# Optimization experiments

Hardware: AMD Instinct MI355X
Metric: run time of the kernel (lower is better)

The kernel has to match this reference:

```python
import jax, jax.numpy as jnp
import numpy as np
from jax import lax

VOCAB = 32000
EMB = 512
HID = 1024
BATCH = 64
MAX_LEN = 30
STEPS = MAX_LEN + 2
SOS = 1
PAD = 0


def setup_inputs() -> dict:
    key = jax.random.key(0)
    ks = jax.random.split(key, 9)
    s = 0.05
    target = jax.random.randint(ks[0], (BATCH, 1), 0, VOCAB)
    encoder_hidden = jax.random.normal(ks[1], (1, BATCH, HID), dtype=jnp.float32)
    emb = jax.random.normal(ks[2], (VOCAB, EMB), dtype=jnp.float32) * s
    emb = emb.at[PAD].set(0.0)  # padding_idx row zeroed like torch
    W_ih = jax.random.normal(ks[3], (3 * HID, EMB), dtype=jnp.float32) * s
    W_hh = jax.random.normal(ks[4], (3 * HID, HID), dtype=jnp.float32) * s
    b_ih = jax.random.normal(ks[5], (3 * HID,), dtype=jnp.float32) * s
    b_hh = jax.random.normal(ks[6], (3 * HID,), dtype=jnp.float32) * s
    fc_W = jax.random.normal(ks[7], (VOCAB, HID), dtype=jnp.float32) * s
    fc_b = jax.random.normal(ks[8], (VOCAB,), dtype=jnp.float32) * s
    return {"target": target, "encoder_hidden": encoder_hidden, "emb": emb,
            "W_ih": W_ih, "W_hh": W_hh, "b_ih": b_ih, "b_hh": b_hh,
            "fc_W": fc_W, "fc_b": fc_b}


def reference(target, encoder_hidden, emb, W_ih, W_hh, b_ih, b_hh, fc_W, fc_b):
    B = target.shape[0]

    def step(carry, _):
        tok, h = carry                      # tok [B] int, h [B,H]
        x = emb[tok]                        # [B,E] embedding lookup
        gi = x @ W_ih.T + b_ih              # [B,3H]
        gh = h @ W_hh.T + b_hh              # [B,3H]
        i_r, i_z, i_n = jnp.split(gi, 3, axis=-1)
        h_r, h_z, h_n = jnp.split(gh, 3, axis=-1)
        r = jax.nn.sigmoid(i_r + h_r)
        z = jax.nn.sigmoid(i_z + h_z)
        n = jnp.tanh(i_n + r * h_n)
        h_new = (1.0 - z) * n + z * h       # torch GRU update
        logits = h_new @ fc_W.T + fc_b      # [B,V]
        logp = jax.nn.log_softmax(logits, axis=-1)
        tok_new = jnp.argmax(logp, axis=-1)  # greedy feedback (topk, k=1)
        return (tok_new, h_new), logp

    h0 = encoder_hidden[0]                  # num_layers == 1
    tok0 = jnp.full((B,), SOS, dtype=jnp.int32)
    (_, hT), outs = lax.scan(step, (tok0, h0), None, length=STEPS)
    decoder_outputs = jnp.transpose(outs, (1, 0, 2))  # [B, STEPS, V]
    return decoder_outputs, hT[None]
```

## Files before the change

kernel.cpp:

```cpp
#include <hip/hip_runtime.h>

#define VV 32000
#define EE 512
#define HH 1024
#define NB 64
#define NSTEP 32

typedef __attribute__((ext_vector_type(8))) short short8;
typedef __attribute__((ext_vector_type(4))) float f32x4;
typedef unsigned long long u64;

#define MFMA16(a, b, c) __builtin_amdgcn_mfma_f32_16x16x32_bf16((a), (b), (c), 0, 0, 0)

__device__ __forceinline__ unsigned short f2bf(float f) {
  unsigned int u = __float_as_uint(f);
  u += 0x7fffu + ((u >> 16) & 1u);
  return (unsigned short)(u >> 16);
}
__device__ __forceinline__ float bf2f(unsigned short b) {
  return __uint_as_float(((unsigned int)b) << 16);
}
__device__ __forceinline__ float sigmoidf_(float x) { return 1.0f / (1.0f + expf(-x)); }
__device__ __forceinline__ unsigned int ordkey(float f) {
  unsigned int u = __float_as_uint(f);
  return u ^ ((u >> 31) ? 0xFFFFFFFFu : 0x80000000u);
}
__device__ __forceinline__ float ordkey_inv(unsigned int u) {
  return __uint_as_float((u & 0x80000000u) ? (u ^ 0x80000000u) : ~u);
}

__global__ __launch_bounds__(256) void prep_wcat(const float* __restrict__ Wih,
                                                 const float* __restrict__ Whh,
                                                 unsigned short* __restrict__ wm,
                                                 unsigned short* __restrict__ wr) {
  int ub = blockIdx.x / 3, g = blockIdx.x % 3;
  for (int e = threadIdx.x; e < 48 * 64; e += 256) {
    int ks = e >> 6, lane = e & 63;
    int row = g * HH + ub * 16 + (lane & 15);
    int k0 = ks * 32 + ((lane >> 4) << 3);
    const float* srcp = (k0 < EE) ? (Wih + (size_t)row * EE + k0)
                                  : (Whh + (size_t)row * HH + (k0 - EE));
    float4 f0 = ((const float4*)srcp)[0];
    float4 f1 = ((const float4*)srcp)[1];
    float fs[8] = {f0.x, f0.y, f0.z, f0.w, f1.x, f1.y, f1.z, f1.w};
    short8 om, orr;
#pragma unroll
    for (int j = 0; j < 8; ++j) {
      unsigned short m_ = f2bf(fs[j]);
      om[j] = (short)m_;
      orr[j] = (short)f2bf(fs[j] - bf2f(m_));
    }
    size_t o8 = ((size_t)(ub * 3 + g) * 48 + ks) * 64 + lane;
    ((short8*)wm)[o8] = om;
    ((short8*)wr)[o8] = orr;
  }
}

__global__ __launch_bounds__(256) void prep_wfc(const float* __restrict__ fcW,
                                                unsigned short* __restrict__ wfc) {
  int vg = blockIdx.x;
  for (int e = threadIdx.x; e < 4096; e += 256) {
    int ks = e >> 7, n = (e >> 6) & 1, lane = e & 63;
    int v = vg * 32 + n * 16 + (lane & 15);
    int k0 = ks * 32 + ((lane >> 4) << 3);
    const float4* src = (const float4*)(fcW + (size_t)v * HH + k0);
    float4 f0 = src[0];
    float4 f1 = src[1];
    float fs[8] = {f0.x, f0.y, f0.z, f0.w, f1.x, f1.y, f1.z, f1.w};
    short8 o;
#pragma unroll
    for (int j = 0; j < 8; ++j) o[j] = (short)f2bf(fs[j]);
    ((short8*)wfc)[(size_t)((vg * 32 + ks) * 2 + n) * 64 + lane] = o;
  }
}

__global__ __launch_bounds__(256) void init_kernel(
    const float* __restrict__ enc, const float* __restrict__ emb, float* __restrict__ h4a,
    unsigned short* __restrict__ ham, unsigned short* __restrict__ har,
    unsigned short* __restrict__ xam, unsigned short* __restrict__ xar,
    int* __restrict__ cnt, int* __restrict__ arrive) {
  int i = blockIdx.x * 256 + threadIdx.x;
  int b = i >> 10, u = i & 1023;
  float hv = enc[i];
  h4a[i] = hv;
  unsigned short m_ = f2bf(hv);
  size_t idx = (((size_t)(b >> 4) * 32 + (u >> 5)) * 64 + ((b & 15) + (((u >> 3) & 3) << 4))) * 8 + (u & 7);
  ham[idx] = m_;
  har[idx] = f2bf(hv - bf2f(m_));
  if (i < NB * EE) {
    int b2 = i >> 9, k = i & 511;
    float xv = emb[EE + k];
    unsigned short xm = f2bf(xv);
    size_t xi = (((size_t)(b2 >> 4) * 16 + (k >> 5)) * 64 + ((b2 & 15) + (((k >> 3) & 3) << 4))) * 8 + (k & 7);
    xam[xi] = xm;
    xar[xi] = f2bf(xv - bf2f(xm));
  }
  if (i < NB) { cnt[i] = 0; arrive[i] = 0; }
}

__global__ __launch_bounds__(768, 3) void gru_kernel(
    const unsigned short* __restrict__ xam, const unsigned short* __restrict__ xar,
    const unsigned short* __restrict__ him, const unsigned short* __restrict__ hir,
    const float* __restrict__ h4in, float* __restrict__ h4out,
    const unsigned short* __restrict__ wm, const unsigned short* __restrict__ wrs,
    const float* __restrict__ bih, const float* __restrict__ bhh,
    unsigned short* __restrict__ hom, unsigned short* __restrict__ hor) {
  __shared__ float red[12][16][65];
  const int tid = threadIdx.x, lane = tid & 63, w = tid >> 6;
  const int ub = blockIdx.x >> 2, mg = blockIdx.x & 3;
  f32x4 aR{}, aZ{}, aNX{}, aNH{};
  const short8* XM = (const short8*)xam;
  const short8* XR = (const short8*)xar;
  const short8* HM = (const short8*)him;
  const short8* HR = (const short8*)hir;
  const short8* WM = (const short8*)wm;
  const short8* WR = (const short8*)wrs;
#pragma unroll
  for (int s = 0; s < 4; ++s) {
    int ks = w * 4 + s;
    short8 am, ar;
    if (ks < 16) {
      int o = (mg * 16 + ks) * 64 + lane;
      am = XM[o]; ar = XR[o];
    } else {
      int o = (mg * 32 + (ks - 16)) * 64 + lane;
      am = HM[o]; ar = HR[o];
    }
    {
      int o = ((ub * 3 + 0) * 48 + ks) * 64 + lane;
      short8 wmv = WM[o], wrv = WR[o];
      aR = MFMA16(am, wmv, aR); aR = MFMA16(ar, wmv, aR); aR = MFMA16(am, wrv, aR);
    }
    {
      int o = ((ub * 3 + 1) * 48 + ks) * 64 + lane;
      short8 wmv = WM[o], wrv = WR[o];
      aZ = MFMA16(am, wmv, aZ); aZ = MFMA16(ar, wmv, aZ); aZ = MFMA16(am, wrv, aZ);
    }
    {
      int o = ((ub * 3 + 2) * 48 + ks) * 64 + lane;
      short8 wmv = WM[o], wrv = WR[o];
      if (ks < 16) {
        aNX = MFMA16(am, wmv, aNX); aNX = MFMA16(ar, wmv, aNX); aNX = MFMA16(am, wrv, aNX);
      } else {
        aNH = MFMA16(am, wmv, aNH); aNH = MFMA16(ar, wmv, aNH); aNH = MFMA16(am, wrv, aNH);
      }
    }
  }
#pragma unroll
  for (int reg = 0; reg < 4; ++reg) {
    int rr = ((lane >> 4) << 2) + reg, c = lane & 15;
    red[w][rr][c] = aR[reg];
    red[w][rr][16 + c] = aZ[reg];
    red[w][rr][32 + c] = aNX[reg];
    red[w][rr][48 + c] = aNH[reg];
  }
  __syncthreads();
  if (tid < 256) {
    const int mrow = tid >> 4, uu = tid & 15;
    float R = 0.f, Z = 0.f, NX = 0.f, NH = 0.f;
#pragma unroll
    for (int q = 0; q < 12; ++q) {
      R += red[q][mrow][uu];
      Z += red[q][mrow][16 + uu];
      NX += red[q][mrow][32 + uu];
      NH += red[q][mrow][48 + uu];
    }
    const int b = mg * 16 + mrow, u = ub * 16 + uu;
    float r = sigmoidf_(R + bih[u] + bhh[u]);
    float z = sigmoidf_(Z + bih[HH + u] + bhh[HH + u]);
    float n = tanhf(NX + bih[2 * HH + u] + r * (NH + bhh[2 * HH + u]));
    float hold = h4in[b * HH + u];
    float hn = (1.0f - z) * n + z * hold;
    h4out[b * HH + u] = hn;
    unsigned short m_ = f2bf(hn);
    size_t idx = (((size_t)(b >> 4) * 32 + (u >> 5)) * 64 + ((b & 15) + (((u >> 3) & 3) << 4))) * 8 + (u & 7);
    hom[idx] = m_;
    hor[idx] = f2bf(hn - bf2f(m_));
  }
}

__global__ __launch_bounds__(256, 8) void fc_kernel(
    const unsigned short* __restrict__ ham,
    const unsigned short* __restrict__ wfc, const float* __restrict__ fcb,
    unsigned short* __restrict__ lgb, u64* __restrict__ blkkeys, int t) {
  const int tid = threadIdx.x;
  const int lane = tid & 63, w = tid >> 6;
  const int vg = blockIdx.x;
  f32x4 acc0{}, acc1{};
  const short8* HM = (const short8*)ham + (size_t)w * 2048;
  const short8* W = (const short8*)wfc + (size_t)vg * 4096;
#pragma unroll 8
  for (int ks = 0; ks < 32; ++ks) {
    short8 am = HM[ks * 64 + lane];
    short8 w0 = W[(ks * 2 + 0) * 64 + lane];
    short8 w1 = W[(ks * 2 + 1) * 64 + lane];
    acc0 = MFMA16(am, w0, acc0);
    acc1 = MFMA16(am, w1, acc1);
  }
  const int r0 = lane >> 4, c0 = lane & 15;
  const float b0 = fcb[vg * 32 + c0];
  const float b1 = fcb[vg * 32 + 16 + c0];
  u64 kk[4];
#pragma unroll
  for (int reg = 0; reg < 4; ++reg) {
    const int b = w * 16 + r0 * 4 + reg;
    float v0 = acc0[reg] + b0;
    float v1 = acc1[reg] + b1;
    size_t ro = ((size_t)b * NSTEP + t) * VV + (size_t)vg * 32 + c0;
    lgb[ro] = f2bf(v0);
    lgb[ro + 16] = f2bf(v1);
    u64 k0 = ((u64)ordkey(v0) << 32) | (u64)(0xFFFFFFFFu - (unsigned)(vg * 32 + c0));
    u64 k1 = ((u64)ordkey(v1) << 32) | (u64)(0xFFFFFFFFu - (unsigned)(vg * 32 + 16 + c0));
    kk[reg] = k0 > k1 ? k0 : k1;
  }
#pragma unroll
  for (int d = 1; d < 16; d <<= 1)
#pragma unroll
    for (int reg = 0; reg < 4; ++reg) {
      u64 o = __shfl_xor(kk[reg], d, 64);
      if (o > kk[reg]) kk[reg] = o;
    }
  if (c0 == 0) {
#pragma unroll
    for (int reg = 0; reg < 4; ++reg)
      blkkeys[(size_t)(w * 16 + r0 * 4 + reg) * 1000 + vg] = kk[reg];
  }
}

__global__ __launch_bounds__(256) void sel_kernel(
    const unsigned short* __restrict__ lgb, const u64* __restrict__ blkkeys,
    int* __restrict__ cnt, int* __restrict__ cand, int* __restrict__ arrive,
    const float* __restrict__ fcW, const float* __restrict__ fcb,
    const float* __restrict__ emb, const float* __restrict__ h4,
    unsigned short* __restrict__ xam, unsigned short* __restrict__ xar, int t) {
  const int b = blockIdx.x >> 3, q = blockIdx.x & 7;
  const int tid = threadIdx.x;
  __shared__ u64 skey[256];
  __shared__ int slast, stok;
  __shared__ u64 rkey[256];

  const u64* kb = blkkeys + (size_t)b * 1000;
  u64 mk = 0;
  for (int i = tid; i < 1000; i += 256) {
    u64 k = kb[i];
    if (k > mk) mk = k;
  }
  skey[tid] = mk;
  __syncthreads();
  for (int off = 128; off > 0; off >>= 1) {
    if (tid < off && skey[tid + off] > skey[tid]) skey[tid] = skey[tid + off];
    __syncthreads();
  }
  const float Mf = ordkey_inv((unsigned)(skey[0] >> 32));
  const float thr = Mf - 0.10f;

  const short8* r8v = (const short8*)(lgb + ((size_t)b * NSTEP + t) * VV);
  for (int i = q * 500 + tid; i < (q + 1) * 500; i += 256) {
    short8 v8 = r8v[i];
#pragma unroll
    for (int e = 0; e < 8; ++e) {
      float x = bf2f((unsigned short)v8[e]);
      if (x >= thr) {
        int p = atomicAdd(&cnt[b], 1);
        if (p < 256) atomicExch(&cand[b * 256 + p], i * 8 + e);
      }
    }
  }
  __syncthreads();
  if (tid == 0) slast = (atomicAdd(&arrive[b], 1) == 7) ? 1 : 0;
  __syncthreads();
  if (!slast) return;

  int n = atomicAdd(&cnt[b], 0);
  if (n > 256) n = 256;
  const int w = tid >> 6, ln = tid & 63;
  for (int ci = w; ci < n; ci += 4) {
    int v = atomicAdd(&cand[b * 256 + ci], 0);
    float p = 0.f;
#pragma unroll
    for (int qq = 0; qq < 16; ++qq)
      p += h4[b * HH + ln + (qq << 6)] * fcW[(size_t)v * HH + ln + (qq << 6)];
#pragma unroll
    for (int d = 1; d < 64; d <<= 1) p += __shfl_xor(p, d);
    if (ln == 0)
      rkey[ci] = ((u64)ordkey(p + fcb[v]) << 32) | (u64)(0xFFFFFFFFu - (unsigned)v);
  }
  __syncthreads();
  if (tid == 0) {
    u64 bk = 0;
    for (int ci = 0; ci < n; ++ci)
      if (rkey[ci] > bk) bk = rkey[ci];
    stok = (int)(0xFFFFFFFFu - (unsigned)(bk & 0xFFFFFFFFu));
    atomicExch(&cnt[b], 0);
    atomicExch(&arrive[b], 0);
  }
  __syncthreads();

  const int tok = stok;
  for (int k = tid; k < EE; k += 256) {
    float xv = emb[(size_t)tok * EE + k];
    unsigned short xm = f2bf(xv);
    size_t xi = (((size_t)(b >> 4) * 16 + (k >> 5)) * 64 + ((b & 15) + (((k >> 3) & 3) << 4))) * 8 + (k & 7);
    xam[xi] = xm;
    xar[xi] = f2bf(xv - bf2f(xm));
  }
}

__global__ __launch_bounds__(256) void lsm_kernel(const unsigned short* __restrict__ lgb,
                                                  const float* __restrict__ h4,
                                                  float* __restrict__ out) {
  const int bid = blockIdx.x;
  const int tid = threadIdx.x;
  if (bid >= 2048) {
    int i = (bid - 2048) * 256 + tid;
    out[(size_t)NB * NSTEP * VV + i] = h4[i];
    return;
  }
  const short8* r8v = (const short8*)(lgb + (size_t)bid * VV);
  float* orow = out + (size_t)bid * VV;
  __shared__ float mred[256], sred[256];

  float m = -INFINITY;
  for (int i = tid; i < VV / 8; i += 256) {
    short8 v8 = r8v[i];
    float m0 = fmaxf(bf2f((unsigned short)v8[0]), bf2f((unsigned short)v8[1]));
    float m1 = fmaxf(bf2f((unsigned short)v8[2]), bf2f((unsigned short)v8[3]));
    float m2 = fmaxf(bf2f((unsigned short)v8[4]), bf2f((unsigned short)v8[5]));
    float m3 = fmaxf(bf2f((unsigned short)v8[6]), bf2f((unsigned short)v8[7]));
    m = fmaxf(m, fmaxf(fmaxf(m0, m1), fmaxf(m2, m3)));
  }
  mred[tid] = m;
  __syncthreads();
  for (int off = 128; off > 0; off >>= 1) {
    if (tid < off) mred[tid] = fmaxf(mred[tid], mred[tid + off]);
    __syncthreads();
  }
  const float M = mred[0];

  float s0 = 0.f, s1 = 0.f, s2 = 0.f, s3 = 0.f;
  for (int i = tid; i < VV / 8; i += 256) {
    short8 v8 = r8v[i];
    s0 += __expf(bf2f((unsigned short)v8[0]) - M) + __expf(bf2f((unsigned short)v8[4]) - M);
    s1 += __expf(bf2f((unsigned short)v8[1]) - M) + __expf(bf2f((unsigned short)v8[5]) - M);
    s2 += __expf(bf2f((unsigned short)v8[2]) - M) + __expf(bf2f((unsigned short)v8[6]) - M);
    s3 += __expf(bf2f((unsigned short)v8[3]) - M) + __expf(bf2f((unsigned short)v8[7]) - M);
  }
  sred[tid] = (s0 + s1) + (s2 + s3);
  __syncthreads();
  for (int off = 128; off > 0; off >>= 1) {
    if (tid < off) sred[tid] += sred[tid + off];
    __syncthreads();
  }
  const float lse = M + logf(sred[0]);

  for (int i = tid; i < VV / 8; i += 256) {
    short8 v8 = r8v[i];
    float4 o0, o1;
    o0.x = bf2f((unsigned short)v8[0]) - lse;
    o0.y = bf2f((unsigned short)v8[1]) - lse;
    o0.z = bf2f((unsigned short)v8[2]) - lse;
    o0.w = bf2f((unsigned short)v8[3]) - lse;
    o1.x = bf2f((unsigned short)v8[4]) - lse;
    o1.y = bf2f((unsigned short)v8[5]) - lse;
    o1.z = bf2f((unsigned short)v8[6]) - lse;
    o1.w = bf2f((unsigned short)v8[7]) - lse;
    ((float4*)orow)[i * 2] = o0;
    ((float4*)orow)[i * 2 + 1] = o1;
  }
}

extern "C" void kernel_launch(void* const* d_in, const int* in_sizes, int n_in,
                              void* d_out, int out_size, void* d_ws, size_t ws_size,
                              hipStream_t stream) {
  const float* enc = (const float*)d_in[1];
  const float* emb = (const float*)d_in[2];
  const float* Wih = (const float*)d_in[3];
  const float* Whh = (const float*)d_in[4];
  const float* bih = (const float*)d_in[5];
  const float* bhh = (const float*)d_in[6];
  const float* fcW = (const float*)d_in[7];
  const float* fcb = (const float*)d_in[8];
  float* out = (float*)d_out;

  char* ws = (char*)d_ws;
  unsigned short* wfc = (unsigned short*)ws; ws += (size_t)32768000 * 2;
  unsigned short* wcm = (unsigned short*)ws; ws += (size_t)4718592 * 2;
  unsigned short* wcr = (unsigned short*)ws; ws += (size_t)4718592 * 2;
  unsigned short* hAm = (unsigned short*)ws; ws += (size_t)65536 * 2;
  unsigned short* hAr = (unsigned short*)ws; ws += (size_t)65536 * 2;
  unsigned short* hBm = (unsigned short*)ws; ws += (size_t)65536 * 2;
  unsigned short* hBr = (unsigned short*)ws; ws += (size_t)65536 * 2;
  unsigned short* xam = (unsigned short*)ws; ws += (size_t)32768 * 2;
  unsigned short* xar = (unsigned short*)ws; ws += (size_t)32768 * 2;
  float* h4a = (float*)ws; ws += (size_t)NB * HH * 4;
  float* h4b = (float*)ws; ws += (size_t)NB * HH * 4;
  u64* blkkeys = (u64*)ws; ws += (size_t)NB * 1000 * 8;
  int* cnt = (int*)ws; ws += (size_t)NB * 4;
  int* arrive = (int*)ws; ws += (size_t)NB * 4;
  int* cand = (int*)ws; ws += (size_t)NB * 256 * 4;
  unsigned short* lgb = (unsigned short*)ws; ws += (size_t)NB * NSTEP * VV * 2;

  prep_wfc<<<1000, 256, 0, stream>>>(fcW, wfc);
  prep_wcat<<<192, 256, 0, stream>>>(Wih, Whh, wcm, wcr);
  init_kernel<<<256, 256, 0, stream>>>(enc, emb, h4a, hAm, hAr, xam, xar, cnt, arrive);

  for (int t = 0; t < NSTEP; ++t) {
    const float* hin = (t & 1) ? h4b : h4a;
    float* hout = (t & 1) ? h4a : h4b;
    const unsigned short* him = (t & 1) ? hBm : hAm;
    const unsigned short* hir = (t & 1) ? hBr : hAr;
    unsigned short* hom = (t & 1) ? hAm : hBm;
    unsigned short* hor = (t & 1) ? hAr : hBr;
    gru_kernel<<<256, 768, 0, stream>>>(xam, xar, him, hir, hin, hout, wcm, wcr, bih, bhh, hom, hor);
    fc_kernel<<<1000, 256, 0, stream>>>(hom, wfc, fcb, lgb, blkkeys, t);
    sel_kernel<<<512, 256, 0, stream>>>(lgb, blkkeys, cnt, cand, arrive, fcW, fcb, emb, hout, xam, xar, t);
  }
  lsm_kernel<<<2304, 256, 0, stream>>>(lgb, h4a, out);
}
```

Baseline: 1.661 ms.

## Fuse selection into FC kernel using last-arriving blocks per step

The separate selection kernel is folded into the FC projection kernel. Each block bumps a per-step arrival counter, and the last 64 blocks to arrive each take one batch row. Such a block waits until all 1000 blocks have arrived, then does the threshold scan over the full vocab row, rescoring of candidates and embedding gather, keeping candidates in shared memory instead of global atomics. This removes one kernel launch per step and the global candidate and counter traffic. In exchange, 64 blocks now each scan a 32000-entry row alone instead of eight blocks sharing it, and the spin-wait relies on every block of the grid being resident or finishing.

```diff
diff --git a/kernel.cpp b/kernel.cpp
--- a/kernel.cpp
+++ b/kernel.cpp
@@ -78,7 +78,7 @@
     const float* __restrict__ enc, const float* __restrict__ emb, float* __restrict__ h4a,
     unsigned short* __restrict__ ham, unsigned short* __restrict__ har,
     unsigned short* __restrict__ xam, unsigned short* __restrict__ xar,
-    int* __restrict__ cnt, int* __restrict__ arrive) {
+    int* __restrict__ arrive) {
   int i = blockIdx.x * 256 + threadIdx.x;
   int b = i >> 10, u = i & 1023;
   float hv = enc[i];
@@ -95,7 +95,7 @@
     xam[xi] = xm;
     xar[xi] = f2bf(xv - bf2f(xm));
   }
-  if (i < NB) { cnt[i] = 0; arrive[i] = 0; }
+  if (i < NSTEP) arrive[i] = 0;
 }
 
 __global__ __launch_bounds__(768, 3) void gru_kernel(
@@ -179,65 +179,77 @@
   }
 }
 
-__global__ __launch_bounds__(256, 8) void fc_kernel(
+__global__ __launch_bounds__(256, 8) void fcsel_kernel(
     const unsigned short* __restrict__ ham,
     const unsigned short* __restrict__ wfc, const float* __restrict__ fcb,
-    unsigned short* __restrict__ lgb, u64* __restrict__ blkkeys, int t) {
+    unsigned short* __restrict__ lgb, u64* __restrict__ blkkeys,
+    int* __restrict__ arrive,
+    const float* __restrict__ fcW, const float* __restrict__ emb,
+    const float* __restrict__ h4,
+    unsigned short* __restrict__ xam, unsigned short* __restrict__ xar, int t) {
   const int tid = threadIdx.x;
   const int lane = tid & 63, w = tid >> 6;
   const int vg = blockIdx.x;
-  f32x4 acc0{}, acc1{};
-  const short8* HM = (const short8*)ham + (size_t)w * 2048;
-  const short8* W = (const short8*)wfc + (size_t)vg * 4096;
+  __shared__ u64 skey[256];
+  __shared__ u64 rkey[256];
+  __shared__ int scand[256];
+  __shared__ int sint[3];
+
+  {
+    f32x4 acc0{}, acc1{};
+    const short8* HM = (const short8*)ham + (size_t)w * 2048;
+    const short8* W = (const short8*)wfc + (size_t)vg * 4096;
 #pragma unroll 8
-  for (int ks = 0; ks < 32; ++ks) {
-    short8 am = HM[ks * 64 + lane];
-    short8 w0 = W[(ks * 2 + 0) * 64 + lane];
-    short8 w1 = W[(ks * 2 + 1) * 64 + lane];
-    acc0 = MFMA16(am, w0, acc0);
-    acc1 = MFMA16(am, w1, acc1);
-  }
-  const int r0 = lane >> 4, c0 = lane & 15;
-  const float b0 = fcb[vg * 32 + c0];
-  const float b1 = fcb[vg * 32 + 16 + c0];
-  u64 kk[4];
-#pragma unroll
-  for (int reg = 0; reg < 4; ++reg) {
-    const int b = w * 16 + r0 * 4 + reg;
-    float v0 = acc0[reg] + b0;
-    float v1 = acc1[reg] + b1;
-    size_t ro = ((size_t)b * NSTEP + t) * VV + (size_t)vg * 32 + c0;
-    lgb[ro] = f2bf(v0);
-    lgb[ro + 16] = f2bf(v1);
-    u64 k0 = ((u64)ordkey(v0) << 32) | (u64)(0xFFFFFFFFu - (unsigned)(vg * 32 + c0));
-    u64 k1 = ((u64)ordkey(v1) << 32) | (u64)(0xFFFFFFFFu - (unsigned)(vg * 32 + 16 + c0));
-    kk[reg] = k0 > k1 ? k0 : k1;
-  }
-#pragma unroll
-  for (int d = 1; d < 16; d <<= 1)
+    for (int ks = 0; ks < 32; ++ks) {
+      short8 am = HM[ks * 64 + lane];
+      short8 w0 = W[(ks * 2 + 0) * 64 + lane];
+      short8 w1 = W[(ks * 2 + 1) * 64 + lane];
+      acc0 = MFMA16(am, w0, acc0);
+      acc1 = MFMA16(am, w1, acc1);
+    }
+    const int r0 = lane >> 4, c0 = lane & 15;
+    const float b0 = fcb[vg * 32 + c0];
+    const float b1 = fcb[vg * 32 + 16 + c0];
+    u64 kk[4];
 #pragma unroll
     for (int reg = 0; reg < 4; ++reg) {
-      u64 o = __shfl_xor(kk[reg], d, 64);
-      if (o > kk[reg]) kk[reg] = o;
-    }
-  if (c0 == 0) {
-#pragma unroll
-    for (int reg = 0; reg < 4; ++reg)
-      blkkeys[(size_t)(w * 16 + r0 * 4 + reg) * 1000 + vg] = kk[reg];
-  }
-}
-
-__global__ __launch_bounds__(256) void sel_kernel(
-    const unsigned short* __restrict__ lgb, const u64* __restrict__ blkkeys,
-    int* __restrict__ cnt, int* __restrict__ cand, int* __restrict__ arrive,
-    const float* __restrict__ fcW, const float* __restrict__ fcb,
-    const float* __restrict__ emb, const float* __restrict__ h4,
-    unsigned short* __restrict__ xam, unsigned short* __restrict__ xar, int t) {
-  const int b = blockIdx.x >> 3, q = blockIdx.x & 7;
-  const int tid = threadIdx.x;
-  __shared__ u64 skey[256];
-  __shared__ int slast, stok;
-  __shared__ u64 rkey[256];
+      const int b = w * 16 + r0 * 4 + reg;
+      float v0 = acc0[reg] + b0;
+      float v1 = acc1[reg] + b1;
+      size_t ro = ((size_t)b * NSTEP + t) * VV + (size_t)vg * 32 + c0;
+      lgb[ro] = f2bf(v0);
+      lgb[ro + 16] = f2bf(v1);
+      u64 k0 = ((u64)ordkey(v0) << 32) | (u64)(0xFFFFFFFFu - (unsigned)(vg * 32 + c0));
+      u64 k1 = ((u64)ordkey(v1) << 32) | (u64)(0xFFFFFFFFu - (unsigned)(vg * 32 + 16 + c0));
+      kk[reg] = k0 > k1 ? k0 : k1;
+    }
+#pragma unroll
+    for (int d = 1; d < 16; d <<= 1)
+#pragma unroll
+      for (int reg = 0; reg < 4; ++reg) {
+        u64 o = __shfl_xor(kk[reg], d, 64);
+        if (o > kk[reg]) kk[reg] = o;
+      }
+    if (c0 == 0) {
+#pragma unroll
+      for (int reg = 0; reg < 4; ++reg)
+        blkkeys[(size_t)(w * 16 + r0 * 4 + reg) * 1000 + vg] = kk[reg];
+    }
+  }
+
+  __threadfence();
+  __syncthreads();
+  if (tid == 0) sint[0] = atomicAdd(&arrive[t], 1);
+  __syncthreads();
+  const int pos = sint[0];
+  if (pos < 1000 - NB) return;
+  const int b = pos - (1000 - NB);
+
+  if (tid == 0) {
+    while (atomicAdd(&arrive[t], 0) < 1000) { __builtin_amdgcn_s_sleep(8); }
+  }
+  __syncthreads();
+  __threadfence();
 
   const u64* kb = blkkeys + (size_t)b * 1000;
   u64 mk = 0;
@@ -253,29 +265,26 @@
   }
   const float Mf = ordkey_inv((unsigned)(skey[0] >> 32));
   const float thr = Mf - 0.10f;
+  if (tid == 0) sint[1] = 0;
+  __syncthreads();
 
   const short8* r8v = (const short8*)(lgb + ((size_t)b * NSTEP + t) * VV);
-  for (int i = q * 500 + tid; i < (q + 1) * 500; i += 256) {
+  for (int i = tid; i < 4000; i += 256) {
     short8 v8 = r8v[i];
 #pragma unroll
     for (int e = 0; e < 8; ++e) {
       float x = bf2f((unsigned short)v8[e]);
       if (x >= thr) {
-        int p = atomicAdd(&cnt[b], 1);
-        if (p < 256) atomicExch(&cand[b * 256 + p], i * 8 + e);
+        int p = atomicAdd(&sint[1], 1);
+        if (p < 256) scand[p] = i * 8 + e;
       }
     }
   }
   __syncthreads();
-  if (tid == 0) slast = (atomicAdd(&arrive[b], 1) == 7) ? 1 : 0;
-  __syncthreads();
-  if (!slast) return;
-
-  int n = atomicAdd(&cnt[b], 0);
-  if (n > 256) n = 256;
-  const int w = tid >> 6, ln = tid & 63;
-  for (int ci = w; ci < n; ci += 4) {
-    int v = atomicAdd(&cand[b * 256 + ci], 0);
+  int n = sint[1] < 256 ? sint[1] : 256;
+  const int wv_ = tid >> 6, ln = tid & 63;
+  for (int ci = wv_; ci < n; ci += 4) {
+    int v = scand[ci];
     float p = 0.f;
 #pragma unroll
     for (int qq = 0; qq < 16; ++qq)
@@ -290,13 +299,11 @@
     u64 bk = 0;
     for (int ci = 0; ci < n; ++ci)
       if (rkey[ci] > bk) bk = rkey[ci];
-    stok = (int)(0xFFFFFFFFu - (unsigned)(bk & 0xFFFFFFFFu));
-    atomicExch(&cnt[b], 0);
-    atomicExch(&arrive[b], 0);
-  }
-  __syncthreads();
-
-  const int tok = stok;
+    sint[2] = (int)(0xFFFFFFFFu - (unsigned)(bk & 0xFFFFFFFFu));
+  }
+  __syncthreads();
+
+  const int tok = sint[2];
   for (int k = tid; k < EE; k += 256) {
     float xv = emb[(size_t)tok * EE + k];
     unsigned short xm = f2bf(xv);
@@ -395,14 +402,12 @@
   float* h4a = (float*)ws; ws += (size_t)NB * HH * 4;
   float* h4b = (float*)ws; ws += (size_t)NB * HH * 4;
   u64* blkkeys = (u64*)ws; ws += (size_t)NB * 1000 * 8;
-  int* cnt = (int*)ws; ws += (size_t)NB * 4;
-  int* arrive = (int*)ws; ws += (size_t)NB * 4;
-  int* cand = (int*)ws; ws += (size_t)NB * 256 * 4;
+  int* arrive = (int*)ws; ws += (size_t)NSTEP * 4;
   unsigned short* lgb = (unsigned short*)ws; ws += (size_t)NB * NSTEP * VV * 2;
 
   prep_wfc<<<1000, 256, 0, stream>>>(fcW, wfc);
   prep_wcat<<<192, 256, 0, stream>>>(Wih, Whh, wcm, wcr);
-  init_kernel<<<256, 256, 0, stream>>>(enc, emb, h4a, hAm, hAr, xam, xar, cnt, arrive);
+  init_kernel<<<256, 256, 0, stream>>>(enc, emb, h4a, hAm, hAr, xam, xar, arrive);
 
   for (int t = 0; t < NSTEP; ++t) {
     const float* hin = (t & 1) ? h4b : h4a;
@@ -412,8 +417,8 @@
     unsigned short* hom = (t & 1) ? hAm : hBm;
     unsigned short* hor = (t & 1) ? hAr : hBr;
     gru_kernel<<<256, 768, 0, stream>>>(xam, xar, him, hir, hin, hout, wcm, wcr, bih, bhh, hom, hor);
-    fc_kernel<<<1000, 256, 0, stream>>>(hom, wfc, fcb, lgb, blkkeys, t);
-    sel_kernel<<<512, 256, 0, stream>>>(lgb, blkkeys, cnt, cand, arrive, fcW, fcb, emb, hout, xam, xar, t);
+    fcsel_kernel<<<1000, 256, 0, stream>>>(hom, wfc, fcb, lgb, blkkeys, arrive,
+                                           fcW, emb, hout, xam, xar, t);
   }
   lsm_kernel<<<2304, 256, 0, stream>>>(lgb, h4a, out);
 }
```

After: 5.726 ms. +244.7%, slower.
